# Kernel optimization log

Measured on AMD Instinct MI355X. Metric: run time of the kernel, lower is better.

## Reference

```python
import math
import jax, jax.numpy as jnp
import numpy as np

B, S, D, H = 64, 577, 768, 12
DH = D // H          # 64 per-head dim
FF = 4 * D           # 3072 intermediate
EPS = 1e-6


def layernorm(x, g, b):
    mu = jnp.mean(x, axis=-1, keepdims=True)
    var = jnp.mean(jnp.square(x - mu), axis=-1, keepdims=True)
    return (x - mu) * jax.lax.rsqrt(var + EPS) * g + b


def gelu_tanh(x):
    # NewGELUActivation: 0.5*x*(1+tanh(sqrt(2/pi)*(x+0.044715*x^3)))
    c = math.sqrt(2.0 / math.pi)
    return 0.5 * x * (1.0 + jnp.tanh(c * (x + 0.044715 * x ** 3)))


def setup_inputs() -> dict:
    key = jax.random.key(0)
    ks = jax.random.split(key, 16)
    s_d = 1.0 / math.sqrt(D)
    s_ff = 1.0 / math.sqrt(FF)
    return {
        "x": jax.random.normal(ks[0], (B, S, D), jnp.float32),
        "ln1_g": jnp.ones((D,), jnp.float32),
        "ln1_b": jnp.zeros((D,), jnp.float32),
        # per-head Q/K/V weights stacked: [H, D, DH] (equivalent to H separate Linears)
        "Wq": jax.random.normal(ks[1], (H, D, DH), jnp.float32) * s_d,
        "bq": jax.random.normal(ks[2], (H, DH), jnp.float32) * 0.01,
        "Wk": jax.random.normal(ks[3], (H, D, DH), jnp.float32) * s_d,
        "bk": jax.random.normal(ks[4], (H, DH), jnp.float32) * 0.01,
        "Wv": jax.random.normal(ks[5], (H, D, DH), jnp.float32) * s_d,
        "bv": jax.random.normal(ks[6], (H, DH), jnp.float32) * 0.01,
        "Wo": jax.random.normal(ks[7], (D, D), jnp.float32) * s_d,
        "bo": jax.random.normal(ks[8], (D,), jnp.float32) * 0.01,
        "ln2_g": jnp.ones((D,), jnp.float32),
        "ln2_b": jnp.zeros((D,), jnp.float32),
        "W1": jax.random.normal(ks[9], (D, FF), jnp.float32) * s_d,
        "b1": jax.random.normal(ks[10], (FF,), jnp.float32) * 0.01,
        "W2": jax.random.normal(ks[11], (FF, D), jnp.float32) * s_ff,
        "b2": jax.random.normal(ks[12], (D,), jnp.float32) * 0.01,
    }


def reference(x, ln1_g, ln1_b, Wq, bq, Wk, bk, Wv, bv, Wo, bo,
              ln2_g, ln2_b, W1, b1, W2, b2):
    # --- pre-norm MHA ---
    h = layernorm(x, ln1_g, ln1_b)                       # [B,S,D]
    q = jnp.einsum('bsd,hde->bhse', h, Wq) + bq[:, None, :]
    k = jnp.einsum('bsd,hde->bhse', h, Wk) + bk[:, None, :]
    v = jnp.einsum('bsd,hde->bhse', h, Wv) + bv[:, None, :]
    scores = jnp.einsum('bhse,bhte->bhst', q, k) / math.sqrt(DH)
    probs = jax.nn.softmax(scores, axis=-1)              # [B,H,S,S]
    attn = jnp.einsum('bhst,bhte->bhse', probs, v)       # [B,H,S,DH]
    # concat heads in head order -> [B,S,H*DH]
    concat = attn.transpose(0, 2, 1, 3).reshape(B, S, H * DH)
    x = x + concat @ Wo + bo
    # --- pre-norm MLP ---
    m = layernorm(x, ln2_g, ln2_b)
    m = gelu_tanh(m @ W1 + b1) @ W2 + b2
    return x + m
```

## Files before the change

kernel.cpp:

```cpp
#include <hip/hip_runtime.h>
#include <stdint.h>

constexpr int BZ   = 64;
constexpr int SEQ  = 577;
constexpr int DM   = 768;
constexpr int NH   = 12;
constexpr int HD   = 64;
constexpr int FFD  = 3072;
constexpr int ROWS = BZ * SEQ;
constexpr int BHN  = BZ * NH;
constexpr int VTS  = 640;

typedef __attribute__((ext_vector_type(8))) short bf16x8;
typedef __attribute__((ext_vector_type(4))) float f32x4;

static __device__ __forceinline__ unsigned short f2bf(float f) {
  union { float f; uint32_t u; } v; v.f = f;
  uint32_t r = (v.u + 0x7FFFu + ((v.u >> 16) & 1u)) >> 16;
  return (unsigned short)r;
}

static __device__ __forceinline__ f32x4 mfma16(bf16x8 a, bf16x8 b, f32x4 c) {
  return __builtin_amdgcn_mfma_f32_16x16x32_bf16(a, b, c, 0, 0, 0);
}

static __device__ __forceinline__ void gload_lds16(const unsigned short* g, unsigned short* l) {
  __builtin_amdgcn_global_load_lds((const __attribute__((address_space(1))) unsigned int*)g,
                                   (__attribute__((address_space(3))) unsigned int*)l, 16, 0, 0);
}

__global__ __launch_bounds__(256) void prep_qkv(const float* __restrict__ Wq,
                                                const float* __restrict__ Wk,
                                                const float* __restrict__ Wv,
                                                unsigned short* __restrict__ dst) {
  int tid = blockIdx.x * 256 + threadIdx.x;
  int n = tid / DM, k = tid - n * DM;
  int seg = n / DM;
  int within = n - seg * DM;
  int h = within >> 6, e = within & 63;
  const float* W = (seg == 0) ? Wq : (seg == 1) ? Wk : Wv;
  dst[tid] = f2bf(W[((size_t)h * DM + k) * HD + e]);
}

__global__ __launch_bounds__(256) void prep_t(const float* __restrict__ src,
                                              unsigned short* __restrict__ dst,
                                              int N, int K) {
  int tid = blockIdx.x * 256 + threadIdx.x;
  if (tid >= N * K) return;
  int n = tid / K, k = tid - n * K;
  dst[tid] = f2bf(src[(size_t)k * N + n]);
}

__global__ __launch_bounds__(256) void ln_bf16(const float* __restrict__ X,
                                               const float* __restrict__ g,
                                               const float* __restrict__ b,
                                               unsigned short* __restrict__ out) {
  int row  = blockIdx.x * 4 + (threadIdx.x >> 6);
  int lane = threadIdx.x & 63;
  const float* x = X + (size_t)row * DM;
  float4 v[3];
  float s = 0.f, s2 = 0.f;
#pragma unroll
  for (int i = 0; i < 3; i++) {
    v[i] = *(const float4*)(x + i * 256 + lane * 4);
    s  += v[i].x + v[i].y + v[i].z + v[i].w;
    s2 += v[i].x * v[i].x + v[i].y * v[i].y + v[i].z * v[i].z + v[i].w * v[i].w;
  }
#pragma unroll
  for (int o = 1; o < 64; o <<= 1) { s += __shfl_xor(s, o); s2 += __shfl_xor(s2, o); }
  float mu  = s * (1.f / DM);
  float var = s2 * (1.f / DM) - mu * mu;
  float inv = rsqrtf(var + 1e-6f);
#pragma unroll
  for (int i = 0; i < 3; i++) {
    int c = i * 256 + lane * 4;
    float4 gg = *(const float4*)(g + c);
    float4 bb = *(const float4*)(b + c);
    ushort4 o4;
    o4.x = f2bf((v[i].x - mu) * inv * gg.x + bb.x);
    o4.y = f2bf((v[i].y - mu) * inv * gg.y + bb.y);
    o4.z = f2bf((v[i].z - mu) * inv * gg.z + bb.z);
    o4.w = f2bf((v[i].w - mu) * inv * gg.w + bb.w);
    *(ushort4*)(out + (size_t)row * DM + c) = o4;
  }
}

template <int EPI>
__global__ __launch_bounds__(256) void gemm_bt(
    const unsigned short* __restrict__ A, const unsigned short* __restrict__ Bt,
    int M, int N, int K, int nbn,
    const float* __restrict__ bias0, const float* __restrict__ bias1,
    const float* __restrict__ bias2, const float* __restrict__ xres,
    float* __restrict__ outf,
    unsigned short* __restrict__ ob0, unsigned short* __restrict__ ob1,
    unsigned short* __restrict__ ob2) {
  __shared__ __align__(16) unsigned short sA[128 * 64];
  __shared__ __align__(16) unsigned short sB[128 * 64];
  const int tid  = threadIdx.x;
  const int wave = tid >> 6;
  const int lane = tid & 63;
  const int l15 = lane & 15, quad = lane >> 4;

  const int nb = gridDim.x;
  const int L = blockIdx.x;
  const int per = nb >> 3, rem = nb & 7;
  const int x8 = L & 7, i8 = L >> 3;
  const int g = x8 * per + (x8 < rem ? x8 : rem) + i8;
  const int mt = g / nbn, nt = g - mt * nbn;
  const int m0 = mt * 128, n0 = nt * 128;
  const int wm = (wave >> 1) * 64, wn = (wave & 1) * 64;

  f32x4 acc[4][4] = {};
  const int nkt = K >> 6;
  for (int kt = 0; kt < nkt; ++kt) {
#pragma unroll
    for (int j = 0; j < 4; j++) {
      int c = tid + j * 256;
      int row = c >> 3, col = c & 7;
      int kc = col ^ (row & 7);
      int ra = m0 + row; if (ra >= M) ra = M - 1;
      gload_lds16(A  + (size_t)ra * K         + (kt << 6) + kc * 8, sA + c * 8);
      gload_lds16(Bt + (size_t)(n0 + row) * K + (kt << 6) + kc * 8, sB + c * 8);
    }
    __syncthreads();
#pragma unroll
    for (int h = 0; h < 2; h++) {
      bf16x8 aF[4], bF[4];
      const int swz = ((h << 2) | quad) ^ (l15 & 7);
#pragma unroll
      for (int mi = 0; mi < 4; mi++) aF[mi] = *(const bf16x8*)(sA + (wm + mi * 16 + l15) * 64 + swz * 8);
#pragma unroll
      for (int ni = 0; ni < 4; ni++) bF[ni] = *(const bf16x8*)(sB + (wn + ni * 16 + l15) * 64 + swz * 8);
#pragma unroll
      for (int mi = 0; mi < 4; mi++)
#pragma unroll
        for (int ni = 0; ni < 4; ni++) acc[mi][ni] = mfma16(aF[mi], bF[ni], acc[mi][ni]);
    }
    __syncthreads();
  }

#pragma unroll
  for (int mi = 0; mi < 4; mi++) {
#pragma unroll
    for (int r = 0; r < 4; r++) {
      int mg = m0 + wm + mi * 16 + quad * 4 + r;
      if (mg >= M) continue;
      if constexpr (EPI == 0) {
        int bb = mg / SEQ, ss = mg - bb * SEQ;
        int seg = n0 / DM;
        int within0 = n0 - seg * DM + wn;
#pragma unroll
        for (int ni = 0; ni < 4; ni++) {
          int wcol = within0 + ni * 16 + l15;
          int h = wcol >> 6, e = wcol & 63;
          float val = acc[mi][ni][r];
          if (seg == 0) {
            float qv = (val + bias0[wcol]) * 0.125f;
            ob0[((size_t)(bb * NH + h) * SEQ + ss) * HD + e] = f2bf(qv);
          } else if (seg == 1) {
            float kv = val + bias1[wcol];
            ob1[((size_t)(bb * NH + h) * SEQ + ss) * HD + e] = f2bf(kv);
          } else {
            float vv = val + bias2[wcol];
            ob2[((size_t)(bb * NH + h) * HD + e) * VTS + ss] = f2bf(vv);
          }
        }
      } else if constexpr (EPI == 1) {
        size_t base = (size_t)mg * DM;
#pragma unroll
        for (int ni = 0; ni < 4; ni++) {
          int col = n0 + wn + ni * 16 + l15;
          outf[base + col] = xres[base + col] + acc[mi][ni][r] + bias0[col];
        }
      } else if constexpr (EPI == 2) {
        size_t base = (size_t)mg * FFD;
#pragma unroll
        for (int ni = 0; ni < 4; ni++) {
          int col = n0 + wn + ni * 16 + l15;
          float xv = acc[mi][ni][r] + bias0[col];
          float u  = 0.7978845608028654f * (xv + 0.044715f * xv * xv * xv);
          float uc = fminf(fmaxf(u, -15.f), 15.f);
          float t  = __expf(2.f * uc);
          float gel = 0.5f * xv * (1.f + (t - 1.f) / (t + 1.f));
          ob0[base + col] = f2bf(gel);
        }
      } else {
        size_t base = (size_t)mg * DM;
#pragma unroll
        for (int ni = 0; ni < 4; ni++) {
          int col = n0 + wn + ni * 16 + l15;
          outf[base + col] += acc[mi][ni][r] + bias0[col];
        }
      }
    }
  }
}

__global__ __launch_bounds__(256) void attn_fused(
    const unsigned short* __restrict__ Q, const unsigned short* __restrict__ Kb,
    const unsigned short* __restrict__ Vt, unsigned short* __restrict__ Cc) {
  __shared__ __align__(16) unsigned short sK[64 * 72];
  __shared__ __align__(16) unsigned short sV[64 * 72];
  __shared__ __align__(16) unsigned short sP[4][16 * 72];
  const int tid  = threadIdx.x;
  const int wave = tid >> 6, lane = tid & 63;
  const int quad = lane >> 4, l15 = lane & 15;
  const int bh = blockIdx.y;
  const int q0 = blockIdx.x * 64;

  int qr = q0 + wave * 16 + l15; if (qr > SEQ - 1) qr = SEQ - 1;
  const unsigned short* qrow = Q + ((size_t)bh * SEQ + qr) * HD;
  bf16x8 aQ0 = *(const bf16x8*)(qrow + quad * 8);
  bf16x8 aQ1 = *(const bf16x8*)(qrow + 32 + quad * 8);

  float m[4], l[4];
  f32x4 accO[4] = {};
#pragma unroll
  for (int r = 0; r < 4; r++) { m[r] = -3e38f; l[r] = 0.f; }

  for (int t0 = 0; t0 < SEQ; t0 += 64) {
#pragma unroll
    for (int i = 0; i < 2; i++) {
      int c = tid + i * 256;
      int row = c >> 3, col = (c & 7) << 3;
      int tk = t0 + row; if (tk > SEQ - 1) tk = SEQ - 1;
      bf16x8 vk = *(const bf16x8*)(Kb + ((size_t)bh * SEQ + tk) * HD + col);
      bf16x8 vv = *(const bf16x8*)(Vt + ((size_t)bh * HD + row) * VTS + t0 + col);
      *(bf16x8*)(sK + row * 72 + col) = vk;
      *(bf16x8*)(sV + row * 72 + col) = vv;
    }
    __syncthreads();

    f32x4 s4[4];
#pragma unroll
    for (int ni = 0; ni < 4; ni++) {
      bf16x8 b0 = *(const bf16x8*)(sK + (ni * 16 + l15) * 72 + quad * 8);
      bf16x8 b1 = *(const bf16x8*)(sK + (ni * 16 + l15) * 72 + 32 + quad * 8);
      f32x4 a = {0.f, 0.f, 0.f, 0.f};
      a = mfma16(aQ0, b0, a);
      a = mfma16(aQ1, b1, a);
      s4[ni] = a;
    }
#pragma unroll
    for (int ni = 0; ni < 4; ni++) {
      if (t0 + ni * 16 + l15 >= SEQ) {
#pragma unroll
        for (int r = 0; r < 4; r++) s4[ni][r] = -3e38f;
      }
    }
    float mn[4], alpha[4], ts[4];
#pragma unroll
    for (int r = 0; r < 4; r++) {
      float tm = fmaxf(fmaxf(s4[0][r], s4[1][r]), fmaxf(s4[2][r], s4[3][r]));
#pragma unroll
      for (int o = 1; o < 16; o <<= 1) tm = fmaxf(tm, __shfl_xor(tm, o));
      mn[r] = fmaxf(m[r], tm);
      alpha[r] = __expf(m[r] - mn[r]);
      m[r] = mn[r];
      ts[r] = 0.f;
    }
#pragma unroll
    for (int ni = 0; ni < 4; ni++) {
#pragma unroll
      for (int r = 0; r < 4; r++) {
        float p = __expf(s4[ni][r] - mn[r]);
        ts[r] += p;
        sP[wave][(quad * 4 + r) * 72 + ni * 16 + l15] = f2bf(p);
      }
    }
#pragma unroll
    for (int r = 0; r < 4; r++) {
#pragma unroll
      for (int o = 1; o < 16; o <<= 1) ts[r] += __shfl_xor(ts[r], o);
      l[r] = l[r] * alpha[r] + ts[r];
#pragma unroll
      for (int ni = 0; ni < 4; ni++) accO[ni][r] *= alpha[r];
    }
    bf16x8 aP0 = *(const bf16x8*)(sP[wave] + l15 * 72 + quad * 8);
    bf16x8 aP1 = *(const bf16x8*)(sP[wave] + l15 * 72 + 32 + quad * 8);
#pragma unroll
    for (int ni = 0; ni < 4; ni++) {
      bf16x8 v0 = *(const bf16x8*)(sV + (ni * 16 + l15) * 72 + quad * 8);
      bf16x8 v1 = *(const bf16x8*)(sV + (ni * 16 + l15) * 72 + 32 + quad * 8);
      accO[ni] = mfma16(aP0, v0, accO[ni]);
      accO[ni] = mfma16(aP1, v1, accO[ni]);
    }
    __syncthreads();
  }

  int bb = bh / NH, h = bh - bb * NH;
#pragma unroll
  for (int r = 0; r < 4; r++) {
    int ss = q0 + wave * 16 + quad * 4 + r;
    if (ss < SEQ) {
      float inv = 1.f / l[r];
      size_t base = ((size_t)bb * SEQ + ss) * DM + h * HD;
#pragma unroll
      for (int ni = 0; ni < 4; ni++)
        Cc[base + ni * 16 + l15] = f2bf(accO[ni][r] * inv);
    }
  }
}

extern "C" void kernel_launch(void* const* d_in, const int* in_sizes, int n_in,
                              void* d_out, int out_size, void* d_ws, size_t ws_size,
                              hipStream_t stream) {
  (void)in_sizes; (void)n_in; (void)out_size; (void)ws_size;
  const float* x     = (const float*)d_in[0];
  const float* ln1_g = (const float*)d_in[1];
  const float* ln1_b = (const float*)d_in[2];
  const float* Wq    = (const float*)d_in[3];
  const float* bq    = (const float*)d_in[4];
  const float* Wk    = (const float*)d_in[5];
  const float* bk    = (const float*)d_in[6];
  const float* Wv    = (const float*)d_in[7];
  const float* bv    = (const float*)d_in[8];
  const float* Wo    = (const float*)d_in[9];
  const float* bo    = (const float*)d_in[10];
  const float* ln2_g = (const float*)d_in[11];
  const float* ln2_b = (const float*)d_in[12];
  const float* W1    = (const float*)d_in[13];
  const float* b1    = (const float*)d_in[14];
  const float* W2    = (const float*)d_in[15];
  const float* b2    = (const float*)d_in[16];
  float* out = (float*)d_out;

  char* ws = (char*)d_ws;
  size_t off = 0;
  auto alloc = [&](size_t bytes) -> unsigned short* {
    unsigned short* p = (unsigned short*)(ws + off);
    off += (bytes + 255) & ~(size_t)255;
    return p;
  };
  unsigned short* h_bf  = alloc((size_t)ROWS * DM * 2);
  unsigned short* q_bf  = alloc((size_t)BHN * SEQ * HD * 2);
  unsigned short* k_bf  = alloc((size_t)BHN * SEQ * HD * 2);
  unsigned short* vt_bf = alloc((size_t)BHN * HD * VTS * 2);
  unsigned short* cc_bf = alloc((size_t)ROWS * DM * 2);
  unsigned short* g_bf = q_bf;
  unsigned short* wqkv_t = alloc((size_t)2304 * 768 * 2);
  unsigned short* w1_t   = alloc((size_t)3072 * 768 * 2);
  unsigned short* w2_t   = alloc((size_t)768 * 3072 * 2);
  unsigned short* wo_t   = alloc((size_t)768 * 768 * 2);

  prep_qkv<<<(2304 * 768) / 256, 256, 0, stream>>>(Wq, Wk, Wv, wqkv_t);
  prep_t<<<(3072 * 768) / 256, 256, 0, stream>>>(W1, w1_t, 3072, 768);
  prep_t<<<(768 * 3072) / 256, 256, 0, stream>>>(W2, w2_t, 768, 3072);
  prep_t<<<(768 * 768) / 256, 256, 0, stream>>>(Wo, wo_t, 768, 768);

  const int MB = (ROWS + 127) / 128;

  ln_bf16<<<ROWS / 4, 256, 0, stream>>>(x, ln1_g, ln1_b, h_bf);
  gemm_bt<0><<<MB * 18, 256, 0, stream>>>(
      h_bf, wqkv_t, ROWS, 2304, 768, 18, bq, bk, bv, nullptr, nullptr, q_bf, k_bf, vt_bf);
  attn_fused<<<dim3((SEQ + 63) / 64, BHN), 256, 0, stream>>>(q_bf, k_bf, vt_bf, cc_bf);
  gemm_bt<1><<<MB * 6, 256, 0, stream>>>(
      cc_bf, wo_t, ROWS, 768, 768, 6, bo, nullptr, nullptr, x, out, nullptr, nullptr, nullptr);
  ln_bf16<<<ROWS / 4, 256, 0, stream>>>(out, ln2_g, ln2_b, h_bf);
  gemm_bt<2><<<MB * 24, 256, 0, stream>>>(
      h_bf, w1_t, ROWS, 3072, 768, 24, b1, nullptr, nullptr, nullptr, nullptr, g_bf, nullptr, nullptr);
  gemm_bt<3><<<MB * 6, 256, 0, stream>>>(
      g_bf, w2_t, ROWS, 768, 3072, 6, b2, nullptr, nullptr, nullptr, out, nullptr, nullptr, nullptr);
}
```

Baseline: 1.479 ms.

## Rewrite GEMM as 256x256 tile, 8-wave, 4-stage LDS pipelined kernel

Replaces the 128x128 single-buffered GEMM with a 256x256 tile computed by 512 threads (8 waves), using a 4-deep ring of K=32 LDS buffers filled by direct global-to-LDS loads issued three stages ahead. MFMA phases are interleaved with the loads for the next stages, using explicit s_waitcnt, barriers, sched_barrier and setprio to overlap memory traffic with compute. The larger tile raises arithmetic intensity and halves the block count, which may cause tail imbalance on the N=768 GEMMs and increases register pressure with 32 accumulators per lane. Launch grids are updated to match.

```diff
diff --git a/kernel.cpp b/kernel.cpp
--- a/kernel.cpp
+++ b/kernel.cpp
@@ -86,7 +86,7 @@
 }
 
 template <int EPI>
-__global__ __launch_bounds__(256) void gemm_bt(
+__global__ __launch_bounds__(512, 2) void gemm_bt(
     const unsigned short* __restrict__ A, const unsigned short* __restrict__ Bt,
     int M, int N, int K, int nbn,
     const float* __restrict__ bias0, const float* __restrict__ bias1,
@@ -94,12 +94,14 @@
     float* __restrict__ outf,
     unsigned short* __restrict__ ob0, unsigned short* __restrict__ ob1,
     unsigned short* __restrict__ ob2) {
-  __shared__ __align__(16) unsigned short sA[128 * 64];
-  __shared__ __align__(16) unsigned short sB[128 * 64];
+  __shared__ __align__(16) unsigned short sA[4][256 * 32];
+  __shared__ __align__(16) unsigned short sB[4][256 * 32];
   const int tid  = threadIdx.x;
   const int wave = tid >> 6;
   const int lane = tid & 63;
   const int l15 = lane & 15, quad = lane >> 4;
+  const int wmi = wave >> 2;
+  const int wni = wave & 3;
 
   const int nb = gridDim.x;
   const int L = blockIdx.x;
@@ -107,48 +109,99 @@
   const int x8 = L & 7, i8 = L >> 3;
   const int g = x8 * per + (x8 < rem ? x8 : rem) + i8;
   const int mt = g / nbn, nt = g - mt * nbn;
-  const int m0 = mt * 128, n0 = nt * 128;
-  const int wm = (wave >> 1) * 64, wn = (wave & 1) * 64;
-
-  f32x4 acc[4][4] = {};
-  const int nkt = K >> 6;
-  for (int kt = 0; kt < nkt; ++kt) {
-#pragma unroll
-    for (int j = 0; j < 4; j++) {
-      int c = tid + j * 256;
-      int row = c >> 3, col = c & 7;
-      int kc = col ^ (row & 7);
-      int ra = m0 + row; if (ra >= M) ra = M - 1;
-      gload_lds16(A  + (size_t)ra * K         + (kt << 6) + kc * 8, sA + c * 8);
-      gload_lds16(Bt + (size_t)(n0 + row) * K + (kt << 6) + kc * 8, sB + c * 8);
-    }
-    __syncthreads();
-#pragma unroll
-    for (int h = 0; h < 2; h++) {
-      bf16x8 aF[4], bF[4];
-      const int swz = ((h << 2) | quad) ^ (l15 & 7);
-#pragma unroll
-      for (int mi = 0; mi < 4; mi++) aF[mi] = *(const bf16x8*)(sA + (wm + mi * 16 + l15) * 64 + swz * 8);
-#pragma unroll
-      for (int ni = 0; ni < 4; ni++) bF[ni] = *(const bf16x8*)(sB + (wn + ni * 16 + l15) * 64 + swz * 8);
-#pragma unroll
-      for (int mi = 0; mi < 4; mi++)
-#pragma unroll
-        for (int ni = 0; ni < 4; ni++) acc[mi][ni] = mfma16(aF[mi], bF[ni], acc[mi][ni]);
-    }
-    __syncthreads();
-  }
-
-#pragma unroll
-  for (int mi = 0; mi < 4; mi++) {
+  const int m0 = mt * 256, n0 = nt * 256;
+
+  const unsigned short* srcA[2];
+  const unsigned short* srcB[2];
+  int ldsOff[2];
+#pragma unroll
+  for (int j = 0; j < 2; j++) {
+    int c = tid + j * 512;
+    int row = c >> 2, col = c & 3;
+    int kc = col ^ (row & 3);
+    int ra = m0 + row; if (ra >= M) ra = M - 1;
+    srcA[j] = A + (size_t)ra * K + kc * 8;
+    srcB[j] = Bt + (size_t)(n0 + row) * K + kc * 8;
+    ldsOff[j] = c * 8;
+  }
+
+  const int sx8  = (quad ^ (l15 & 3)) * 8;
+  const int offAb = (wmi * 128 + l15) * 32 + sx8;
+  const int offBb = (wni * 64 + l15) * 32 + sx8;
+
+  f32x4 acc[8][4] = {};
+  const int nkt = K >> 5;
+
+#pragma unroll
+  for (int tt = 0; tt < 3; ++tt) {
+#pragma unroll
+    for (int j = 0; j < 2; j++) gload_lds16(srcA[j] + tt * 32, &sA[tt][ldsOff[j]]);
+#pragma unroll
+    for (int j = 0; j < 2; j++) gload_lds16(srcB[j] + tt * 32, &sB[tt][ldsOff[j]]);
+  }
+  asm volatile("s_waitcnt vmcnt(8)" ::: "memory");
+  __builtin_amdgcn_s_barrier();
+
+  for (int t = 0; t < nkt; ++t) {
+    const int rb  = t & 3;
+    const int sbf = (t + 3) & 3;
+    const bool st = (t + 3) < nkt;
+    const size_t koff = (size_t)(t + 3) << 5;
+    const unsigned short* sAr = sA[rb];
+    const unsigned short* sBr = sB[rb];
+
+    bf16x8 aF[4], bF[4];
+#pragma unroll
+    for (int mi = 0; mi < 4; mi++) aF[mi] = *(const bf16x8*)(sAr + offAb + mi * 512);
+#pragma unroll
+    for (int ni = 0; ni < 4; ni++) bF[ni] = *(const bf16x8*)(sBr + offBb + ni * 512);
+    if (st) {
+      gload_lds16(srcA[0] + koff, &sA[sbf][ldsOff[0]]);
+      gload_lds16(srcA[1] + koff, &sA[sbf][ldsOff[1]]);
+    }
+    __builtin_amdgcn_s_barrier();
+    asm volatile("s_waitcnt lgkmcnt(0)" ::: "memory");
+    __builtin_amdgcn_sched_barrier(0);
+    __builtin_amdgcn_s_setprio(1);
+#pragma unroll
+    for (int mi = 0; mi < 4; mi++)
+#pragma unroll
+      for (int ni = 0; ni < 4; ni++) acc[mi][ni] = mfma16(aF[mi], bF[ni], acc[mi][ni]);
+    __builtin_amdgcn_s_setprio(0);
+    __builtin_amdgcn_s_barrier();
+
+    bf16x8 aG[4];
+#pragma unroll
+    for (int mi = 0; mi < 4; mi++) aG[mi] = *(const bf16x8*)(sAr + offAb + (mi + 4) * 512);
+    if (st) {
+      gload_lds16(srcB[0] + koff, &sB[sbf][ldsOff[0]]);
+      gload_lds16(srcB[1] + koff, &sB[sbf][ldsOff[1]]);
+    }
+    __builtin_amdgcn_s_barrier();
+    asm volatile("s_waitcnt lgkmcnt(0)" ::: "memory");
+    __builtin_amdgcn_sched_barrier(0);
+    __builtin_amdgcn_s_setprio(1);
+#pragma unroll
+    for (int mi = 0; mi < 4; mi++)
+#pragma unroll
+      for (int ni = 0; ni < 4; ni++) acc[mi + 4][ni] = mfma16(aG[mi], bF[ni], acc[mi + 4][ni]);
+    __builtin_amdgcn_s_setprio(0);
+    if (st)                   { asm volatile("s_waitcnt vmcnt(8)" ::: "memory"); }
+    else if (t + 2 < nkt)     { asm volatile("s_waitcnt vmcnt(4)" ::: "memory"); }
+    else if (t + 1 < nkt)     { asm volatile("s_waitcnt vmcnt(0)" ::: "memory"); }
+    if (t + 1 < nkt) __builtin_amdgcn_s_barrier();
+  }
+
+#pragma unroll
+  for (int mi = 0; mi < 8; mi++) {
 #pragma unroll
     for (int r = 0; r < 4; r++) {
-      int mg = m0 + wm + mi * 16 + quad * 4 + r;
+      int mg = m0 + wmi * 128 + mi * 16 + quad * 4 + r;
       if (mg >= M) continue;
       if constexpr (EPI == 0) {
         int bb = mg / SEQ, ss = mg - bb * SEQ;
         int seg = n0 / DM;
-        int within0 = n0 - seg * DM + wn;
+        int within0 = n0 - seg * DM + wni * 64;
 #pragma unroll
         for (int ni = 0; ni < 4; ni++) {
           int wcol = within0 + ni * 16 + l15;
@@ -169,14 +222,14 @@
         size_t base = (size_t)mg * DM;
 #pragma unroll
         for (int ni = 0; ni < 4; ni++) {
-          int col = n0 + wn + ni * 16 + l15;
+          int col = n0 + wni * 64 + ni * 16 + l15;
           outf[base + col] = xres[base + col] + acc[mi][ni][r] + bias0[col];
         }
       } else if constexpr (EPI == 2) {
         size_t base = (size_t)mg * FFD;
 #pragma unroll
         for (int ni = 0; ni < 4; ni++) {
-          int col = n0 + wn + ni * 16 + l15;
+          int col = n0 + wni * 64 + ni * 16 + l15;
           float xv = acc[mi][ni][r] + bias0[col];
           float u  = 0.7978845608028654f * (xv + 0.044715f * xv * xv * xv);
           float uc = fminf(fmaxf(u, -15.f), 15.f);
@@ -188,7 +241,7 @@
         size_t base = (size_t)mg * DM;
 #pragma unroll
         for (int ni = 0; ni < 4; ni++) {
-          int col = n0 + wn + ni * 16 + l15;
+          int col = n0 + wni * 64 + ni * 16 + l15;
           outf[base + col] += acc[mi][ni][r] + bias0[col];
         }
       }
@@ -348,17 +401,17 @@
   prep_t<<<(768 * 3072) / 256, 256, 0, stream>>>(W2, w2_t, 768, 3072);
   prep_t<<<(768 * 768) / 256, 256, 0, stream>>>(Wo, wo_t, 768, 768);
 
-  const int MB = (ROWS + 127) / 128;
+  const int MB2 = (ROWS + 255) / 256;
 
   ln_bf16<<<ROWS / 4, 256, 0, stream>>>(x, ln1_g, ln1_b, h_bf);
-  gemm_bt<0><<<MB * 18, 256, 0, stream>>>(
-      h_bf, wqkv_t, ROWS, 2304, 768, 18, bq, bk, bv, nullptr, nullptr, q_bf, k_bf, vt_bf);
+  gemm_bt<0><<<MB2 * 9, 512, 0, stream>>>(
+      h_bf, wqkv_t, ROWS, 2304, 768, 9, bq, bk, bv, nullptr, nullptr, q_bf, k_bf, vt_bf);
   attn_fused<<<dim3((SEQ + 63) / 64, BHN), 256, 0, stream>>>(q_bf, k_bf, vt_bf, cc_bf);
-  gemm_bt<1><<<MB * 6, 256, 0, stream>>>(
-      cc_bf, wo_t, ROWS, 768, 768, 6, bo, nullptr, nullptr, x, out, nullptr, nullptr, nullptr);
+  gemm_bt<1><<<MB2 * 3, 512, 0, stream>>>(
+      cc_bf, wo_t, ROWS, 768, 768, 3, bo, nullptr, nullptr, x, out, nullptr, nullptr, nullptr);
   ln_bf16<<<ROWS / 4, 256, 0, stream>>>(out, ln2_g, ln2_b, h_bf);
-  gemm_bt<2><<<MB * 24, 256, 0, stream>>>(
-      h_bf, w1_t, ROWS, 3072, 768, 24, b1, nullptr, nullptr, nullptr, nullptr, g_bf, nullptr, nullptr);
-  gemm_bt<3><<<MB * 6, 256, 0, stream>>>(
-      g_bf, w2_t, ROWS, 768, 3072, 6, b2, nullptr, nullptr, nullptr, out, nullptr, nullptr, nullptr);
-}
+  gemm_bt<2><<<MB2 * 12, 512, 0, stream>>>(
+      h_bf, w1_t, ROWS, 3072, 768, 12, b1, nullptr, nullptr, nullptr, nullptr, g_bf, nullptr, nullptr);
+  gemm_bt<3><<<MB2 * 3, 512, 0, stream>>>(
+      g_bf, w2_t, ROWS, 768, 3072, 3, b2, nullptr, nullptr, nullptr, out, nullptr, nullptr, nullptr);
+}
```

New measurement: 1.570 ms. +6.2%, slower.
